# Kernel tuning notes

Measured on AMD Instinct MI355X. Metric: run time of the kernel, lower is better.

The kernel has to match this reference:

```python
import jax, jax.numpy as jnp
import numpy as np

B, L, D, H, DFF = 16, 2048, 256, 8, 1024
CYCLES = 2
DEP = D // H
EPS = 1e-6


def _mha(q, k, v, Wq, Wk, Wv, Wo, bo):
    # q: [N, Lq, D], k/v: [N, Lk, D]  (mask is None in the source for both calls)
    N, Lq, _ = q.shape
    Lk = k.shape[1]
    qh = (q @ Wq).reshape(N, Lq, H, DEP)
    kh = (k @ Wk).reshape(N, Lk, H, DEP)
    vh = (v @ Wv).reshape(N, Lk, H, DEP)
    logits = jnp.einsum('nqhd,nkhd->nhqk', qh, kh) / jnp.sqrt(jnp.float32(DEP))
    w = jax.nn.softmax(logits, axis=-1)
    o = jnp.einsum('nhqk,nkhd->nqhd', w, vh).reshape(N, Lq, D)
    return o @ Wo + bo


def _layernorm(x, g, b):
    mu = jnp.mean(x, axis=-1, keepdims=True)
    var = jnp.mean(jnp.square(x - mu), axis=-1, keepdims=True)
    return g * (x - mu) * jax.lax.rsqrt(var + EPS) + b


def setup_inputs() -> dict:
    key = jax.random.key(0)
    ks = jax.random.split(key, 10)
    sc = 1.0 / np.sqrt(D)
    return {
        'e': jax.random.normal(ks[0], (B, L, D), dtype=jnp.float32),
        'Wq': jax.random.normal(ks[1], (D, D), dtype=jnp.float32) * sc,
        'Wk': jax.random.normal(ks[2], (D, D), dtype=jnp.float32) * sc,
        'Wv': jax.random.normal(ks[3], (D, D), dtype=jnp.float32) * sc,
        'Wo': jax.random.normal(ks[4], (D, D), dtype=jnp.float32) * sc,
        'bo': jnp.zeros((D,), dtype=jnp.float32),
        'W1': jax.random.normal(ks[5], (D, DFF), dtype=jnp.float32) * sc,
        'b1': jnp.zeros((DFF,), dtype=jnp.float32),
        'W2': jax.random.normal(ks[6], (DFF, D), dtype=jnp.float32) * (1.0 / np.sqrt(DFF)),
        'b2': jnp.zeros((D,), dtype=jnp.float32),
        'g1': jnp.ones((D,), dtype=jnp.float32),
        'be1': jnp.zeros((D,), dtype=jnp.float32),
        'g2': jnp.ones((D,), dtype=jnp.float32),
        'be2': jnp.zeros((D,), dtype=jnp.float32),
        'training': False,
    }


def reference(e, Wq, Wk, Wv, Wo, bo, W1, b1, W2, b2, g1, be1, g2, be2, training):
    # training=False -> dropouts are identity (eval mode)
    b, l, d = e.shape
    h = e
    s = jnp.mean(h, axis=1)  # relay node [b, d]
    for _ in range(CYCLES):
        h_last = jnp.roll(h, -1, axis=1)  # cycle_shift(h, False)
        h_next = jnp.roll(h, 1, axis=1)   # cycle_shift(h, True)
        s_m = jnp.broadcast_to(s[:, None, :], h.shape)
        # context [b, l, 5, d] -> [b*l, 5, d]
        c = jnp.stack([h_last, h, h_next, e, s_m], axis=-2).reshape(b * l, 5, d)
        hq = h.reshape(b * l, 1, d)
        h = jax.nn.relu(_mha(hq, c, c, Wq, Wk, Wv, Wo, bo)).reshape(b, l, d)
        # relay attention (the source reuses multi_att_satellite weights here)
        sq = s[:, None, :]               # [b, 1, d]
        mc = jnp.concatenate([sq, h], axis=1)  # [b, l+1, d]
        s = jax.nn.relu(_mha(sq, mc, mc, Wq, Wk, Wv, Wo, bo)).reshape(b, d)
    out1 = _layernorm(e + h, g1, be1)
    ffn = jax.nn.relu(out1 @ W1 + b1) @ W2 + b2
    out2 = _layernorm(out1 + ffn, g2, be2)
    return out2, s
```

## Files before the change

### kernel.cpp

```cpp
#include <hip/hip_runtime.h>

typedef unsigned short u16;
typedef unsigned int u32;
typedef __attribute__((ext_vector_type(8))) short bf16x8;
typedef __attribute__((ext_vector_type(4))) float f32x4;

#define LCONST __launch_bounds__(256)

__device__ __forceinline__ u16 f2bf(float f) {
  u32 u = __float_as_uint(f);
  u32 r = (u + 0x7FFFu + ((u >> 16) & 1u)) >> 16;
  return (u16)r;
}
__device__ __forceinline__ float bflo(u32 w) { return __uint_as_float(w << 16); }
__device__ __forceinline__ float bfhi(u32 w) { return __uint_as_float(w & 0xFFFF0000u); }
__device__ __forceinline__ float b2f(u16 v) { return __uint_as_float(((u32)v) << 16); }

__device__ __forceinline__ float dot8(uint4 u, const float* q) {
  return q[0]*bflo(u.x) + q[1]*bfhi(u.x) + q[2]*bflo(u.y) + q[3]*bfhi(u.y)
       + q[4]*bflo(u.z) + q[5]*bfhi(u.z) + q[6]*bflo(u.w) + q[7]*bfhi(u.w);
}
__device__ __forceinline__ void fma8(uint4 u, float wt, float* a) {
  a[0] = fmaf(wt, bflo(u.x), a[0]); a[1] = fmaf(wt, bfhi(u.x), a[1]);
  a[2] = fmaf(wt, bflo(u.y), a[2]); a[3] = fmaf(wt, bfhi(u.y), a[3]);
  a[4] = fmaf(wt, bflo(u.z), a[4]); a[5] = fmaf(wt, bfhi(u.z), a[5]);
  a[6] = fmaf(wt, bflo(u.w), a[6]); a[7] = fmaf(wt, bfhi(u.w), a[7]);
}

__device__ __forceinline__ void gload16(const u16* g, u16* l) {
  __builtin_amdgcn_global_load_lds(
      (const __attribute__((address_space(1))) unsigned int*)g,
      (__attribute__((address_space(3))) unsigned int*)l, 16, 0, 0);
}

__global__ LCONST void prep_kernel(const float* __restrict__ e,
                                   const float* __restrict__ Wq, const float* __restrict__ Wk,
                                   const float* __restrict__ Wv, const float* __restrict__ Wo,
                                   const float* __restrict__ W1, const float* __restrict__ W2,
                                   u16* __restrict__ Wqkv_t, u16* __restrict__ Wo_t,
                                   u16* __restrict__ W1_t, u16* __restrict__ W2_t,
                                   float* __restrict__ part, u16* __restrict__ ebf) {
  int blk = blockIdx.x;
  int tid = threadIdx.x;
  if (blk < 3072) {
    int idx = blk * 256 + tid;
    if (idx < 196608) {
      int sub = idx >> 16, r = idx & 65535;
      int n = r >> 8, k = r & 255;
      const float* src = (sub == 0) ? Wq : ((sub == 1) ? Wk : Wv);
      Wqkv_t[idx] = f2bf(src[(size_t)k * 256 + n]);
    } else if (idx < 262144) {
      int r = idx - 196608;
      int n = r >> 8, k = r & 255;
      Wo_t[r] = f2bf(Wo[(size_t)k * 256 + n]);
    } else if (idx < 524288) {
      int r = idx - 262144;
      int n = r >> 8, k = r & 255;
      W1_t[r] = f2bf(W1[(size_t)k * 1024 + n]);
    } else {
      int r = idx - 524288;
      int n = r >> 10, k = r & 1023;
      W2_t[r] = f2bf(W2[(size_t)k * 256 + n]);
    }
  } else {
    int mb = blk - 3072;
    int b = mb >> 5, c = mb & 31;
    size_t base = ((size_t)b * 2048 + (size_t)c * 64) * 256 + tid;
    float s = 0.f;
    #pragma unroll 8
    for (int i = 0; i < 64; i++) {
      float v = e[base + (size_t)i * 256];
      s += v;
      ebf[base + (size_t)i * 256] = f2bf(v);
    }
    part[(size_t)mb * 256 + tid] = s;
  }
}

template <int BM, int BN, int EPI>
__global__ __launch_bounds__(512, (BM == 128) ? 4 : 6)
void gemm3_kernel(const u16* __restrict__ A, const u16* __restrict__ Bt,
                  const float* __restrict__ bias,
                  u16* __restrict__ C0, u16* __restrict__ C1, u16* __restrict__ C2,
                  const u16* __restrict__ resbf,
                  const float* __restrict__ g, const float* __restrict__ be,
                  float* __restrict__ Fout,
                  int M, int N, int K) {
  constexpr int WR = BM / 2;
  constexpr int MR = WR / 16;
  constexpr int ACH_PW = (BM / 8) / 8;
  constexpr int BCH_PW = 4;
  __shared__ __align__(16) u16 As[BM * 64];
  __shared__ __align__(16) u16 Bs[BN * 64];

  const int tid = threadIdx.x, lane = tid & 63, wid = tid >> 6;
  const int wm = wid >> 2, wn = wid & 3;

  const int ncol = N / BN;
  const int nwg = gridDim.x;
  const int bid = blockIdx.x;
  const int swz = (bid & 7) * (nwg >> 3) + (bid >> 3);
  const int mb = swz / ncol, nb = swz - mb * ncol;
  const int m0 = mb * BM, n0 = nb * BN;

  const int lrow8 = lane >> 3;
  const int cg = (lane & 7) ^ lrow8;

  f32x4 acc[MR][4] = {};
  for (int kt = 0; kt < K; kt += 64) {
    #pragma unroll
    for (int it = 0; it < ACH_PW; it++) {
      int ca = wid * ACH_PW + it;
      int row = ca * 8 + lrow8;
      gload16(A + (size_t)(m0 + row) * K + kt + cg * 8, (u16*)As + ca * 512);
    }
    #pragma unroll
    for (int it = 0; it < BCH_PW; it++) {
      int cb = wid * BCH_PW + it;
      int row = cb * 8 + lrow8;
      gload16(Bt + (size_t)(n0 + row) * K + kt + cg * 8, (u16*)Bs + cb * 512);
    }
    __syncthreads();
    const int lr = lane & 15, hi = lane >> 4;
    #pragma unroll
    for (int kk = 0; kk < 2; kk++) {
      const int slot = (kk * 4 + hi) ^ (lr & 7);
      bf16x8 af[MR], bfr[4];
      #pragma unroll
      for (int m = 0; m < MR; m++)
        af[m] = *(const bf16x8*)&As[(wm * WR + m * 16 + lr) * 64 + slot * 8];
      #pragma unroll
      for (int n = 0; n < 4; n++)
        bfr[n] = *(const bf16x8*)&Bs[(wn * 64 + n * 16 + lr) * 64 + slot * 8];
      #pragma unroll
      for (int m = 0; m < MR; m++)
        #pragma unroll
        for (int n = 0; n < 4; n++)
          acc[m][n] = __builtin_amdgcn_mfma_f32_16x16x32_bf16(af[m], bfr[n], acc[m][n], 0, 0, 0);
    }
    __syncthreads();
  }

  const int lr = lane & 15, hi = lane >> 4;
  if constexpr (EPI == 0) {
    const int bsel = n0 >> 8;
    u16* C = (bsel == 0) ? C0 : ((bsel == 1) ? C1 : C2);
    #pragma unroll
    for (int m = 0; m < MR; m++)
      #pragma unroll
      for (int n = 0; n < 4; n++)
        #pragma unroll
        for (int r = 0; r < 4; r++) {
          int row = m0 + wm * WR + m * 16 + hi * 4 + r;
          int col = wn * 64 + n * 16 + lr;
          C[(size_t)row * 256 + col] = f2bf(acc[m][n][r]);
        }
  } else if constexpr (EPI == 1) {
    #pragma unroll
    for (int m = 0; m < MR; m++)
      #pragma unroll
      for (int n = 0; n < 4; n++)
        #pragma unroll
        for (int r = 0; r < 4; r++) {
          int row = m0 + wm * WR + m * 16 + hi * 4 + r;
          int col = n0 + wn * 64 + n * 16 + lr;
          float v = fmaxf(acc[m][n][r] + bias[col], 0.f);
          C0[(size_t)row * N + col] = f2bf(v);
        }
  } else {
    __shared__ float rsum[BM], rsq[BM];
    if (tid < BM) { rsum[tid] = 0.f; rsq[tid] = 0.f; }
    __syncthreads();
    #pragma unroll
    for (int m = 0; m < MR; m++)
      #pragma unroll
      for (int n = 0; n < 4; n++)
        #pragma unroll
        for (int r = 0; r < 4; r++) {
          int rl = wm * WR + m * 16 + hi * 4 + r;
          int col = wn * 64 + n * 16 + lr;
          size_t gi = (size_t)(m0 + rl) * 256 + col;
          float v = acc[m][n][r] + bias[col];
          float x;
          if constexpr (EPI == 2) {
            v = fmaxf(v, 0.f);
            C0[gi] = f2bf(v);
            x = b2f(resbf[gi]) + v;
          } else {
            x = b2f(resbf[gi]) + v;
          }
          acc[m][n][r] = x;
        }
    #pragma unroll
    for (int m = 0; m < MR; m++)
      #pragma unroll
      for (int r = 0; r < 4; r++) {
        float s = 0.f, q = 0.f;
        #pragma unroll
        for (int n = 0; n < 4; n++) { float x = acc[m][n][r]; s += x; q += x * x; }
        #pragma unroll
        for (int off = 1; off < 16; off <<= 1) {
          s += __shfl_xor(s, off);
          q += __shfl_xor(q, off);
        }
        if (lr == 0) {
          int rl = wm * WR + m * 16 + hi * 4 + r;
          atomicAdd(&rsum[rl], s);
          atomicAdd(&rsq[rl], q);
        }
      }
    __syncthreads();
    #pragma unroll
    for (int m = 0; m < MR; m++)
      #pragma unroll
      for (int n = 0; n < 4; n++)
        #pragma unroll
        for (int r = 0; r < 4; r++) {
          int rl = wm * WR + m * 16 + hi * 4 + r;
          int col = wn * 64 + n * 16 + lr;
          size_t gi = (size_t)(m0 + rl) * 256 + col;
          float mu = rsum[rl] * (1.f / 256.f);
          float var = rsq[rl] * (1.f / 256.f) - mu * mu;
          float rstd = rsqrtf(fmaxf(var, 0.f) + 1e-6f);
          float o = g[col] * (acc[m][n][r] - mu) * rstd + be[col];
          if constexpr (EPI == 2) C1[gi] = f2bf(o);
          else                    Fout[gi] = o;
        }
  }
}

template <bool MEAN>
__global__ LCONST void proj_kernel(const float* __restrict__ X, const float* __restrict__ part,
                                   const float* __restrict__ Wq, const float* __restrict__ Wk,
                                   const float* __restrict__ Wv, float* __restrict__ Yq,
                                   float* __restrict__ Yk, float* __restrict__ Yv) {
  __shared__ float xs[256];
  __shared__ float red[256];
  const int b = blockIdx.x;
  const int wsel = blockIdx.y >> 2, n0 = (blockIdx.y & 3) * 64;
  const int tid = threadIdx.x;
  if constexpr (MEAN) {
    float s = 0.f;
    #pragma unroll
    for (int c = 0; c < 32; c++) s += part[((size_t)b * 32 + c) * 256 + tid];
    xs[tid] = s * (1.f / 2048.f);
  } else {
    xs[tid] = X[b * 256 + tid];
  }
  __syncthreads();
  const float* W = (wsel == 0) ? Wq : ((wsel == 1) ? Wk : Wv);
  float* Y = (wsel == 0) ? Yq : ((wsel == 1) ? Yk : Yv);
  const int c = tid & 63, g = tid >> 6;
  float p = 0.f;
  #pragma unroll 8
  for (int j = g * 64; j < g * 64 + 64; j++)
    p = fmaf(xs[j], W[(size_t)j * 256 + n0 + c], p);
  red[tid] = p;
  __syncthreads();
  if (g == 0)
    Y[b * 256 + n0 + c] = red[c] + red[64 + c] + red[128 + c] + red[192 + c];
}

__global__ LCONST void attn1_kernel(const u16* __restrict__ hq, const u16* __restrict__ pk,
                                    const u16* __restrict__ pv, const u16* __restrict__ ek,
                                    const u16* __restrict__ ev, const float* __restrict__ skp,
                                    const float* __restrict__ svp, u16* __restrict__ outp) {
  int t = blockIdx.x * 256 + threadIdx.x;
  int h = t & 7;
  size_t token = (size_t)(t >> 3);
  int b = (int)(token >> 11);
  int i = (int)(token & 2047);
  size_t tb = (size_t)b << 11;
  size_t ip = tb + ((i + 1) & 2047);
  size_t im = tb + ((i + 2047) & 2047);
  const int off = h * 32;

  float qf[32];
  {
    const u16* q = hq + token * 256 + off;
    #pragma unroll
    for (int c = 0; c < 4; c++) {
      uint4 u = *(const uint4*)(q + c * 8);
      qf[c*8+0] = bflo(u.x); qf[c*8+1] = bfhi(u.x);
      qf[c*8+2] = bflo(u.y); qf[c*8+3] = bfhi(u.y);
      qf[c*8+4] = bflo(u.z); qf[c*8+5] = bfhi(u.z);
      qf[c*8+6] = bflo(u.w); qf[c*8+7] = bfhi(u.w);
    }
  }
  const u16* kr0 = pk + ip * 256 + off;
  const u16* kr1 = pk + token * 256 + off;
  const u16* kr2 = pk + im * 256 + off;
  const u16* kr3 = ek + token * 256 + off;
  float lg[5];
  {
    float d0 = 0, d1 = 0, d2 = 0, d3 = 0;
    #pragma unroll
    for (int cc = 0; cc < 4; cc++) {
      d0 += dot8(*(const uint4*)(kr0 + cc * 8), qf + cc * 8);
      d1 += dot8(*(const uint4*)(kr1 + cc * 8), qf + cc * 8);
      d2 += dot8(*(const uint4*)(kr2 + cc * 8), qf + cc * 8);
      d3 += dot8(*(const uint4*)(kr3 + cc * 8), qf + cc * 8);
    }
    lg[0] = d0; lg[1] = d1; lg[2] = d2; lg[3] = d3;
    float d4 = 0;
    const float* s = skp + b * 256 + off;
    #pragma unroll
    for (int j = 0; j < 32; j++) d4 = fmaf(qf[j], s[j], d4);
    lg[4] = d4;
  }
  const float sc = 0.17677669529663687f;
  float m = lg[0];
  #pragma unroll
  for (int c = 1; c < 5; c++) m = fmaxf(m, lg[c]);
  float w[5], den = 0.f;
  #pragma unroll
  for (int c = 0; c < 5; c++) { w[c] = __expf((lg[c] - m) * sc); den += w[c]; }

  float a[32];
  #pragma unroll
  for (int j = 0; j < 32; j++) a[j] = 0.f;
  const u16* vr0 = pv + ip * 256 + off;
  const u16* vr1 = pv + token * 256 + off;
  const u16* vr2 = pv + im * 256 + off;
  const u16* vr3 = ev + token * 256 + off;
  #pragma unroll
  for (int cc = 0; cc < 4; cc++) {
    fma8(*(const uint4*)(vr0 + cc * 8), w[0], a + cc * 8);
    fma8(*(const uint4*)(vr1 + cc * 8), w[1], a + cc * 8);
    fma8(*(const uint4*)(vr2 + cc * 8), w[2], a + cc * 8);
    fma8(*(const uint4*)(vr3 + cc * 8), w[3], a + cc * 8);
  }
  {
    const float* s = svp + b * 256 + off;
    #pragma unroll
    for (int j = 0; j < 32; j++) a[j] = fmaf(w[4], s[j], a[j]);
  }
  float inv = 1.f / den;
  u16* o = outp + token * 256 + off;
  #pragma unroll
  for (int c = 0; c < 4; c++) {
    uint4 u;
    u.x = (u32)f2bf(a[c*8+0] * inv) | ((u32)f2bf(a[c*8+1] * inv) << 16);
    u.y = (u32)f2bf(a[c*8+2] * inv) | ((u32)f2bf(a[c*8+3] * inv) << 16);
    u.z = (u32)f2bf(a[c*8+4] * inv) | ((u32)f2bf(a[c*8+5] * inv) << 16);
    u.w = (u32)f2bf(a[c*8+6] * inv) | ((u32)f2bf(a[c*8+7] * inv) << 16);
    *(uint4*)(o + c * 8) = u;
  }
}

__global__ LCONST void mha2a_kernel(const float* __restrict__ sqp, const float* __restrict__ skp,
                                    const float* __restrict__ svp, const u16* __restrict__ pk,
                                    const u16* __restrict__ pv, float* __restrict__ partial) {
  __shared__ float rmax[4], rsum[4], racc[4][32];
  const int blk = blockIdx.x;
  const int bh = blk >> 2, c = blk & 3;
  const int b = bh >> 3, h = bh & 7;
  const int tid = threadIdx.x;
  const int lane = tid & 63, wid = tid >> 6;
  const int off = h * 32;
  const float sc = 0.17677669529663687f;

  float qf[32];
  {
    const float* q = sqp + b * 256 + off;
    #pragma unroll
    for (int j = 0; j < 32; j++) qf[j] = q[j];
  }
  const int k0 = c * 512 + tid;
  const int k1 = k0 + 256;
  const u16* kp0 = pk + ((size_t)b * 2048 + k0) * 256 + off;
  const u16* kp1 = pk + ((size_t)b * 2048 + k1) * 256 + off;
  float d0 = 0.f, d1 = 0.f;
  #pragma unroll
  for (int cc = 0; cc < 4; cc++) {
    d0 += dot8(*(const uint4*)(kp0 + cc * 8), qf + cc * 8);
    d1 += dot8(*(const uint4*)(kp1 + cc * 8), qf + cc * 8);
  }
  d0 *= sc; d1 *= sc;
  float ds = -1e30f;
  if (c == 0 && tid == 0) {
    float d = 0.f;
    const float* k = skp + b * 256 + off;
    #pragma unroll
    for (int j = 0; j < 32; j++) d = fmaf(qf[j], k[j], d);
    ds = d * sc;
  }
  float lmax = fmaxf(fmaxf(d0, d1), ds);
  #pragma unroll
  for (int o = 32; o; o >>= 1) lmax = fmaxf(lmax, __shfl_down(lmax, o));
  if (lane == 0) rmax[wid] = lmax;
  __syncthreads();
  const float M = fmaxf(fmaxf(rmax[0], rmax[1]), fmaxf(rmax[2], rmax[3]));

  float w0 = __expf(d0 - M), w1 = __expf(d1 - M);
  float lsum = w0 + w1;
  float a[32];
  #pragma unroll
  for (int j = 0; j < 32; j++) a[j] = 0.f;
  const u16* vp0 = pv + ((size_t)b * 2048 + k0) * 256 + off;
  const u16* vp1 = pv + ((size_t)b * 2048 + k1) * 256 + off;
  #pragma unroll
  for (int cc = 0; cc < 4; cc++) {
    fma8(*(const uint4*)(vp0 + cc * 8), w0, a + cc * 8);
    fma8(*(const uint4*)(vp1 + cc * 8), w1, a + cc * 8);
  }
  if (c == 0 && tid == 0) {
    float ws = __expf(ds - M);
    lsum += ws;
    const float* v = svp + b * 256 + off;
    #pragma unroll
    for (int j = 0; j < 32; j++) a[j] = fmaf(ws, v[j], a[j]);
  }
  #pragma unroll
  for (int o = 32; o; o >>= 1) lsum += __shfl_down(lsum, o);
  if (lane == 0) rsum[wid] = lsum;
  #pragma unroll
  for (int j = 0; j < 32; j++) {
    float v = a[j];
    #pragma unroll
    for (int o = 32; o; o >>= 1) v += __shfl_down(v, o);
    if (lane == 0) racc[wid][j] = v;
  }
  __syncthreads();
  float* P = partial + (size_t)blk * 36;
  if (tid < 32) {
    P[2 + tid] = racc[0][tid] + racc[1][tid] + racc[2][tid] + racc[3][tid];
    if (tid == 0) {
      P[0] = M;
      P[1] = rsum[0] + rsum[1] + rsum[2] + rsum[3];
    }
  }
}

__global__ LCONST void mha2c_kernel(const float* __restrict__ partial,
                                    const float* __restrict__ Wo, const float* __restrict__ bo,
                                    float* __restrict__ Y) {
  __shared__ float xs[256];
  __shared__ float red[256];
  const int b = blockIdx.x;
  const int n0 = blockIdx.y * 64;
  const int tid = threadIdx.x;
  {
    int hh = tid >> 5, d = tid & 31;
    const float* P = partial + (size_t)(b * 8 + hh) * 144;
    float M = fmaxf(fmaxf(P[0], P[36]), fmaxf(P[72], P[108]));
    float l = 0.f, o = 0.f;
    #pragma unroll
    for (int c = 0; c < 4; c++) {
      float f = __expf(P[c * 36] - M);
      l += f * P[c * 36 + 1];
      o += f * P[c * 36 + 2 + d];
    }
    xs[tid] = o / l;
  }
  __syncthreads();
  const int c = tid & 63, g = tid >> 6;
  float p = 0.f;
  #pragma unroll 8
  for (int j = g * 64; j < g * 64 + 64; j++)
    p = fmaf(xs[j], Wo[(size_t)j * 256 + n0 + c], p);
  red[tid] = p;
  __syncthreads();
  if (g == 0) {
    float v = red[c] + red[64 + c] + red[128 + c] + red[192 + c];
    Y[b * 256 + n0 + c] = fmaxf(v + bo[n0 + c], 0.f);
  }
}

extern "C" void kernel_launch(void* const* d_in, const int* in_sizes, int n_in,
                              void* d_out, int out_size, void* d_ws, size_t ws_size,
                              hipStream_t stream) {
  const float* e   = (const float*)d_in[0];
  const float* Wq  = (const float*)d_in[1];
  const float* Wk  = (const float*)d_in[2];
  const float* Wv  = (const float*)d_in[3];
  const float* Wo  = (const float*)d_in[4];
  const float* bo  = (const float*)d_in[5];
  const float* W1  = (const float*)d_in[6];
  const float* b1  = (const float*)d_in[7];
  const float* W2  = (const float*)d_in[8];
  const float* b2  = (const float*)d_in[9];
  const float* g1  = (const float*)d_in[10];
  const float* be1 = (const float*)d_in[11];
  const float* g2  = (const float*)d_in[12];
  const float* be2 = (const float*)d_in[13];

  char* wsb = (char*)d_ws;
  size_t off = 0;
  auto alc = [&](size_t n) { void* p = wsb + off; off += (n + 255) & ~(size_t)255; return p; };
  u16* Wqkv_t = (u16*)alc(768 * 256 * 2);
  u16* Wo_t   = (u16*)alc(65536 * 2);
  u16* W1_t   = (u16*)alc(262144 * 2);
  u16* W2_t   = (u16*)alc(262144 * 2);
  float* sB    = (float*)alc(4096 * 4);
  float* sqp   = (float*)alc(4096 * 4);
  float* skp   = (float*)alc(4096 * 4);
  float* svp   = (float*)alc(4096 * 4);
  float* partM = (float*)alc(512 * 36 * 4);
  float* part  = (float*)alc(524288);
  const size_t SZ = 16777216;
  u16* hq   = (u16*)alc(SZ);
  u16* ek   = (u16*)alc(SZ);
  u16* ev   = (u16*)alc(SZ);
  u16* pk   = (u16*)alc(SZ);
  u16* pv   = (u16*)alc(SZ);
  u16* ao   = (u16*)alc(SZ);
  u16* hbuf = (u16*)alc(SZ);
  u16* ebf  = (u16*)alc(SZ);
  u16* out1 = (u16*)alc(SZ);
  u16* ffn1 = hq;

  const int M = 32768;
  float* outp  = (float*)d_out;
  float* s_out = outp + 8388608;

  prep_kernel<<<3584, 256, 0, stream>>>(e, Wq, Wk, Wv, Wo, W1, W2,
      Wqkv_t, Wo_t, W1_t, W2_t, part, ebf);

  proj_kernel<true><<<dim3(16, 12), 256, 0, stream>>>(nullptr, part, Wq, Wk, Wv, sqp, skp, svp);
  gemm3_kernel<128, 256, 0><<<768, 512, 0, stream>>>(ebf, Wqkv_t, nullptr, hq, ek, ev,
      nullptr, nullptr, nullptr, nullptr, M, 768, 256);
  attn1_kernel<<<1024, 256, 0, stream>>>(hq, ek, ev, ek, ev, skp, svp, ao);
  gemm3_kernel<64, 256, 1><<<512, 512, 0, stream>>>(ao, Wo_t, bo, hbuf, nullptr, nullptr,
      nullptr, nullptr, nullptr, nullptr, M, 256, 256);
  gemm3_kernel<128, 256, 0><<<768, 512, 0, stream>>>(hbuf, Wqkv_t, nullptr, hq, pk, pv,
      nullptr, nullptr, nullptr, nullptr, M, 768, 256);
  mha2a_kernel<<<512, 256, 0, stream>>>(sqp, skp, svp, pk, pv, partM);
  mha2c_kernel<<<dim3(16, 4), 256, 0, stream>>>(partM, Wo, bo, sB);
  proj_kernel<false><<<dim3(16, 12), 256, 0, stream>>>(sB, nullptr, Wq, Wk, Wv, sqp, skp, svp);

  attn1_kernel<<<1024, 256, 0, stream>>>(hq, pk, pv, ek, ev, skp, svp, ao);
  gemm3_kernel<64, 256, 2><<<512, 512, 0, stream>>>(ao, Wo_t, bo, hbuf, out1, nullptr,
      ebf, g1, be1, nullptr, M, 256, 256);
  gemm3_kernel<128, 256, 0><<<512, 512, 0, stream>>>(hbuf, Wqkv_t + 65536, nullptr, pk, pv, nullptr,
      nullptr, nullptr, nullptr, nullptr, M, 512, 256);
  mha2a_kernel<<<512, 256, 0, stream>>>(sqp, skp, svp, pk, pv, partM);
  mha2c_kernel<<<dim3(16, 4), 256, 0, stream>>>(partM, Wo, bo, s_out);

  gemm3_kernel<128, 256, 1><<<1024, 512, 0, stream>>>(out1, W1_t, b1, ffn1, nullptr, nullptr,
      nullptr, nullptr, nullptr, nullptr, M, 1024, 256);
  gemm3_kernel<64, 256, 4><<<512, 512, 0, stream>>>(ffn1, W2_t, b2, nullptr, nullptr, nullptr,
      out1, g2, be2, outp, M, 256, 1024);
  (void)in_sizes; (void)n_in; (void)out_size; (void)ws_size;
}
```

Baseline: 278.5 us.

## Fuse FFN up-projection, ReLU, down-projection and LayerNorm into one kernel

```diff
diff --git a/kernel.cpp b/kernel.cpp
--- a/kernel.cpp
+++ b/kernel.cpp
@@ -181,14 +181,9 @@
           int col = wn * 64 + n * 16 + lr;
           size_t gi = (size_t)(m0 + rl) * 256 + col;
           float v = acc[m][n][r] + bias[col];
-          float x;
-          if constexpr (EPI == 2) {
-            v = fmaxf(v, 0.f);
-            C0[gi] = f2bf(v);
-            x = b2f(resbf[gi]) + v;
-          } else {
-            x = b2f(resbf[gi]) + v;
-          }
+          v = fmaxf(v, 0.f);
+          C0[gi] = f2bf(v);
+          float x = b2f(resbf[gi]) + v;
           acc[m][n][r] = x;
         }
     #pragma unroll
@@ -223,10 +218,154 @@
           float var = rsq[rl] * (1.f / 256.f) - mu * mu;
           float rstd = rsqrtf(fmaxf(var, 0.f) + 1e-6f);
           float o = g[col] * (acc[m][n][r] - mu) * rstd + be[col];
-          if constexpr (EPI == 2) C1[gi] = f2bf(o);
-          else                    Fout[gi] = o;
-        }
-  }
+          C1[gi] = f2bf(o);
+        }
+  }
+}
+
+__global__ __launch_bounds__(512, 2)
+void ffn_fused_kernel(const u16* __restrict__ out1, const u16* __restrict__ W1_t,
+                      const float* __restrict__ b1, const u16* __restrict__ W2_t,
+                      const float* __restrict__ b2, const float* __restrict__ g,
+                      const float* __restrict__ be, float* __restrict__ Fout) {
+  __shared__ __align__(16) u16 As[128 * 64];
+  __shared__ __align__(16) u16 Bs[256 * 64];
+  __shared__ __align__(16) u16 Cs[128 * 256];
+  const int tid = threadIdx.x, lane = tid & 63, wid = tid >> 6;
+  const int wm = wid >> 2, wn = wid & 3;
+  const int nwg = gridDim.x, bid = blockIdx.x;
+  const int swz = (bid & 7) * (nwg >> 3) + (bid >> 3);
+  const int m0 = swz * 128;
+  const int lrow8 = lane >> 3;
+  const int cg = (lane & 7) ^ lrow8;
+  const int lr = lane & 15, hi = lane >> 4;
+
+  f32x4 acc2[4][4] = {};
+  for (int nb = 0; nb < 4; nb++) {
+    f32x4 acc1[4][4] = {};
+    for (int kt = 0; kt < 4; kt++) {
+      #pragma unroll
+      for (int it = 0; it < 2; it++) {
+        int ca = wid * 2 + it;
+        int row = ca * 8 + lrow8;
+        gload16(out1 + (size_t)(m0 + row) * 256 + kt * 64 + cg * 8, (u16*)As + ca * 512);
+      }
+      #pragma unroll
+      for (int it = 0; it < 4; it++) {
+        int cb = wid * 4 + it;
+        int row = cb * 8 + lrow8;
+        gload16(W1_t + (size_t)(nb * 256 + row) * 256 + kt * 64 + cg * 8, (u16*)Bs + cb * 512);
+      }
+      __syncthreads();
+      #pragma unroll
+      for (int kk = 0; kk < 2; kk++) {
+        const int slot = (kk * 4 + hi) ^ (lr & 7);
+        bf16x8 af[4], bfr[4];
+        #pragma unroll
+        for (int m = 0; m < 4; m++)
+          af[m] = *(const bf16x8*)&As[(wm * 64 + m * 16 + lr) * 64 + slot * 8];
+        #pragma unroll
+        for (int n = 0; n < 4; n++)
+          bfr[n] = *(const bf16x8*)&Bs[(wn * 64 + n * 16 + lr) * 64 + slot * 8];
+        #pragma unroll
+        for (int m = 0; m < 4; m++)
+          #pragma unroll
+          for (int n = 0; n < 4; n++)
+            acc1[m][n] = __builtin_amdgcn_mfma_f32_16x16x32_bf16(af[m], bfr[n], acc1[m][n], 0, 0, 0);
+      }
+      __syncthreads();
+    }
+    #pragma unroll
+    for (int m = 0; m < 4; m++)
+      #pragma unroll
+      for (int n = 0; n < 4; n++)
+        #pragma unroll
+        for (int r = 0; r < 4; r++) {
+          int rl = wm * 64 + m * 16 + hi * 4 + r;
+          int col = wn * 64 + n * 16 + lr;
+          float v = fmaxf(acc1[m][n][r] + b1[nb * 256 + col], 0.f);
+          int s = col >> 3;
+          int sp = (s & 24) | ((s & 7) ^ (rl & 7));
+          Cs[rl * 256 + sp * 8 + (col & 7)] = f2bf(v);
+        }
+    __syncthreads();
+    for (int kt2 = 0; kt2 < 4; kt2++) {
+      #pragma unroll
+      for (int it = 0; it < 4; it++) {
+        int cb = wid * 4 + it;
+        int row = cb * 8 + lrow8;
+        gload16(W2_t + (size_t)row * 1024 + nb * 256 + kt2 * 64 + cg * 8, (u16*)Bs + cb * 512);
+      }
+      __syncthreads();
+      #pragma unroll
+      for (int kk = 0; kk < 2; kk++) {
+        const int j = kk * 4 + hi;
+        bf16x8 af[4], bfr[4];
+        #pragma unroll
+        for (int m = 0; m < 4; m++) {
+          int row = wm * 64 + m * 16 + lr;
+          af[m] = *(const bf16x8*)&Cs[row * 256 + (kt2 * 8 + (j ^ (row & 7))) * 8];
+        }
+        #pragma unroll
+        for (int n = 0; n < 4; n++)
+          bfr[n] = *(const bf16x8*)&Bs[(wn * 64 + n * 16 + lr) * 64 + ((j ^ (lr & 7))) * 8];
+        #pragma unroll
+        for (int m = 0; m < 4; m++)
+          #pragma unroll
+          for (int n = 0; n < 4; n++)
+            acc2[m][n] = __builtin_amdgcn_mfma_f32_16x16x32_bf16(af[m], bfr[n], acc2[m][n], 0, 0, 0);
+      }
+      __syncthreads();
+    }
+  }
+  float* rsum = (float*)As;
+  float* rsq  = rsum + 128;
+  if (tid < 128) { rsum[tid] = 0.f; rsq[tid] = 0.f; }
+  __syncthreads();
+  #pragma unroll
+  for (int m = 0; m < 4; m++)
+    #pragma unroll
+    for (int n = 0; n < 4; n++)
+      #pragma unroll
+      for (int r = 0; r < 4; r++) {
+        int rl = wm * 64 + m * 16 + hi * 4 + r;
+        int col = wn * 64 + n * 16 + lr;
+        size_t gi = (size_t)(m0 + rl) * 256 + col;
+        acc2[m][n][r] = acc2[m][n][r] + b2[col] + b2f(out1[gi]);
+      }
+  #pragma unroll
+  for (int m = 0; m < 4; m++)
+    #pragma unroll
+    for (int r = 0; r < 4; r++) {
+      float s = 0.f, q = 0.f;
+      #pragma unroll
+      for (int n = 0; n < 4; n++) { float x = acc2[m][n][r]; s += x; q += x * x; }
+      #pragma unroll
+      for (int off = 1; off < 16; off <<= 1) {
+        s += __shfl_xor(s, off);
+        q += __shfl_xor(q, off);
+      }
+      if (lr == 0) {
+        int rl = wm * 64 + m * 16 + hi * 4 + r;
+        atomicAdd(&rsum[rl], s);
+        atomicAdd(&rsq[rl], q);
+      }
+    }
+  __syncthreads();
+  #pragma unroll
+  for (int m = 0; m < 4; m++)
+    #pragma unroll
+    for (int n = 0; n < 4; n++)
+      #pragma unroll
+      for (int r = 0; r < 4; r++) {
+        int rl = wm * 64 + m * 16 + hi * 4 + r;
+        int col = wn * 64 + n * 16 + lr;
+        size_t gi = (size_t)(m0 + rl) * 256 + col;
+        float mu = rsum[rl] * (1.f / 256.f);
+        float var = rsq[rl] * (1.f / 256.f) - mu * mu;
+        float rstd = rsqrtf(fmaxf(var, 0.f) + 1e-6f);
+        Fout[gi] = g[col] * (acc2[m][n][r] - mu) * rstd + be[col];
+      }
 }
 
 template <bool MEAN>
@@ -508,7 +647,6 @@
   u16* hbuf = (u16*)alc(SZ);
   u16* ebf  = (u16*)alc(SZ);
   u16* out1 = (u16*)alc(SZ);
-  u16* ffn1 = hq;
 
   const int M = 32768;
   float* outp  = (float*)d_out;
@@ -537,9 +675,6 @@
   mha2a_kernel<<<512, 256, 0, stream>>>(sqp, skp, svp, pk, pv, partM);
   mha2c_kernel<<<dim3(16, 4), 256, 0, stream>>>(partM, Wo, bo, s_out);
 
-  gemm3_kernel<128, 256, 1><<<1024, 512, 0, stream>>>(out1, W1_t, b1, ffn1, nullptr, nullptr,
-      nullptr, nullptr, nullptr, nullptr, M, 1024, 256);
-  gemm3_kernel<64, 256, 4><<<512, 512, 0, stream>>>(ffn1, W2_t, b2, nullptr, nullptr, nullptr,
-      out1, g2, be2, outp, M, 256, 1024);
+  ffn_fused_kernel<<<256, 512, 0, stream>>>(out1, W1_t, b1, W2_t, b2, g2, be2, outp);
   (void)in_sizes; (void)n_in; (void)out_size; (void)ws_size;
 }
```

New measurement: 322.9 us. +15.9%, slower.

## Add persistent-A GEMM looping over N blocks and fuse relay output with projection

Applied to the files above, without the earlier changes.

```diff
diff --git a/kernel.cpp b/kernel.cpp
--- a/kernel.cpp
+++ b/kernel.cpp
@@ -77,8 +77,88 @@
   }
 }
 
+template <int NCOL, int EPI>
+__global__ __launch_bounds__(512, 4)
+void gemmP_kernel(const u16* __restrict__ A, const u16* __restrict__ Bt,
+                  const float* __restrict__ bias,
+                  u16* __restrict__ C0, u16* __restrict__ C1, u16* __restrict__ C2) {
+  __shared__ __align__(16) u16 As[64 * 256];
+  __shared__ __align__(16) u16 Bs[256 * 64];
+  const int tid = threadIdx.x, lane = tid & 63, wid = tid >> 6;
+  const int wm = wid >> 2, wn = wid & 3;
+  const int nwg = gridDim.x, bid = blockIdx.x;
+  const int swz = (bid & 7) * (nwg >> 3) + (bid >> 3);
+  const int m0 = swz * 64;
+  const int lrow8 = lane >> 3;
+  const int cg = (lane & 7) ^ lrow8;
+  const int lr = lane & 15, hi = lane >> 4;
+
+  #pragma unroll
+  for (int kt = 0; kt < 4; kt++) {
+    int row = wid * 8 + lrow8;
+    gload16(A + (size_t)(m0 + row) * 256 + kt * 64 + cg * 8,
+            (u16*)As + kt * 4096 + wid * 512);
+  }
+
+  for (int nb = 0; nb < NCOL; nb++) {
+    f32x4 acc[2][4] = {};
+    for (int kt = 0; kt < 4; kt++) {
+      #pragma unroll
+      for (int it = 0; it < 4; it++) {
+        int cb = wid * 4 + it;
+        int row = cb * 8 + lrow8;
+        gload16(Bt + (size_t)(nb * 256 + row) * 256 + kt * 64 + cg * 8,
+                (u16*)Bs + cb * 512);
+      }
+      __syncthreads();
+      #pragma unroll
+      for (int kk = 0; kk < 2; kk++) {
+        const int slot = (kk * 4 + hi) ^ (lr & 7);
+        bf16x8 af[2], bfr[4];
+        #pragma unroll
+        for (int m = 0; m < 2; m++)
+          af[m] = *(const bf16x8*)&As[kt * 4096 + (wm * 32 + m * 16 + lr) * 64 + slot * 8];
+        #pragma unroll
+        for (int n = 0; n < 4; n++)
+          bfr[n] = *(const bf16x8*)&Bs[(wn * 64 + n * 16 + lr) * 64 + slot * 8];
+        #pragma unroll
+        for (int m = 0; m < 2; m++)
+          #pragma unroll
+          for (int n = 0; n < 4; n++)
+            acc[m][n] = __builtin_amdgcn_mfma_f32_16x16x32_bf16(af[m], bfr[n], acc[m][n], 0, 0, 0);
+      }
+      __syncthreads();
+    }
+    if constexpr (EPI == 0) {
+      u16* C = (nb == 0) ? C0 : ((nb == 1) ? C1 : C2);
+      #pragma unroll
+      for (int m = 0; m < 2; m++)
+        #pragma unroll
+        for (int n = 0; n < 4; n++)
+          #pragma unroll
+          for (int r = 0; r < 4; r++) {
+            int row = m0 + wm * 32 + m * 16 + hi * 4 + r;
+            int col = wn * 64 + n * 16 + lr;
+            C[(size_t)row * 256 + col] = f2bf(acc[m][n][r]);
+          }
+    } else {
+      #pragma unroll
+      for (int m = 0; m < 2; m++)
+        #pragma unroll
+        for (int n = 0; n < 4; n++)
+          #pragma unroll
+          for (int r = 0; r < 4; r++) {
+            int row = m0 + wm * 32 + m * 16 + hi * 4 + r;
+            int col = nb * 256 + wn * 64 + n * 16 + lr;
+            float v = fmaxf(acc[m][n][r] + bias[col], 0.f);
+            C0[(size_t)row * (NCOL * 256) + col] = f2bf(v);
+          }
+    }
+  }
+}
+
 template <int BM, int BN, int EPI>
-__global__ __launch_bounds__(512, (BM == 128) ? 4 : 6)
+__global__ __launch_bounds__(512, 6)
 void gemm3_kernel(const u16* __restrict__ A, const u16* __restrict__ Bt,
                   const float* __restrict__ bias,
                   u16* __restrict__ C0, u16* __restrict__ C1, u16* __restrict__ C2,
@@ -142,20 +222,7 @@
   }
 
   const int lr = lane & 15, hi = lane >> 4;
-  if constexpr (EPI == 0) {
-    const int bsel = n0 >> 8;
-    u16* C = (bsel == 0) ? C0 : ((bsel == 1) ? C1 : C2);
-    #pragma unroll
-    for (int m = 0; m < MR; m++)
-      #pragma unroll
-      for (int n = 0; n < 4; n++)
-        #pragma unroll
-        for (int r = 0; r < 4; r++) {
-          int row = m0 + wm * WR + m * 16 + hi * 4 + r;
-          int col = wn * 64 + n * 16 + lr;
-          C[(size_t)row * 256 + col] = f2bf(acc[m][n][r]);
-        }
-  } else if constexpr (EPI == 1) {
+  if constexpr (EPI == 1) {
     #pragma unroll
     for (int m = 0; m < MR; m++)
       #pragma unroll
@@ -465,6 +532,52 @@
     float v = red[c] + red[64 + c] + red[128 + c] + red[192 + c];
     Y[b * 256 + n0 + c] = fmaxf(v + bo[n0 + c], 0.f);
   }
+}
+
+__global__ LCONST void mha2cp_kernel(const float* __restrict__ partial,
+                                     const float* __restrict__ Wo, const float* __restrict__ bo,
+                                     const float* __restrict__ Wq, const float* __restrict__ Wk,
+                                     const float* __restrict__ Wv,
+                                     float* __restrict__ Yq, float* __restrict__ Yk,
+                                     float* __restrict__ Yv) {
+  __shared__ float xs[256];
+  __shared__ float ss[256];
+  __shared__ float red[256];
+  const int b = blockIdx.x;
+  const int wsel = blockIdx.y >> 2, n0 = (blockIdx.y & 3) * 64;
+  const int tid = threadIdx.x;
+  {
+    int hh = tid >> 5, d = tid & 31;
+    const float* P = partial + (size_t)(b * 8 + hh) * 144;
+    float M = fmaxf(fmaxf(P[0], P[36]), fmaxf(P[72], P[108]));
+    float l = 0.f, o = 0.f;
+    #pragma unroll
+    for (int c = 0; c < 4; c++) {
+      float f = __expf(P[c * 36] - M);
+      l += f * P[c * 36 + 1];
+      o += f * P[c * 36 + 2 + d];
+    }
+    xs[tid] = o / l;
+  }
+  __syncthreads();
+  {
+    float a = 0.f;
+    #pragma unroll 8
+    for (int j = 0; j < 256; j++) a = fmaf(xs[j], Wo[(size_t)j * 256 + tid], a);
+    ss[tid] = fmaxf(a + bo[tid], 0.f);
+  }
+  __syncthreads();
+  const float* W = (wsel == 0) ? Wq : ((wsel == 1) ? Wk : Wv);
+  float* Y = (wsel == 0) ? Yq : ((wsel == 1) ? Yk : Yv);
+  const int c = tid & 63, g = tid >> 6;
+  float p = 0.f;
+  #pragma unroll 8
+  for (int j = g * 64; j < g * 64 + 64; j++)
+    p = fmaf(ss[j], W[(size_t)j * 256 + n0 + c], p);
+  red[tid] = p;
+  __syncthreads();
+  if (g == 0)
+    Y[b * 256 + n0 + c] = red[c] + red[64 + c] + red[128 + c] + red[192 + c];
 }
 
 extern "C" void kernel_launch(void* const* d_in, const int* in_sizes, int n_in,
@@ -492,7 +605,6 @@
   u16* Wo_t   = (u16*)alc(65536 * 2);
   u16* W1_t   = (u16*)alc(262144 * 2);
   u16* W2_t   = (u16*)alc(262144 * 2);
-  float* sB    = (float*)alc(4096 * 4);
   float* sqp   = (float*)alc(4096 * 4);
   float* skp   = (float*)alc(4096 * 4);
   float* svp   = (float*)alc(4096 * 4);
@@ -518,27 +630,22 @@
       Wqkv_t, Wo_t, W1_t, W2_t, part, ebf);
 
   proj_kernel<true><<<dim3(16, 12), 256, 0, stream>>>(nullptr, part, Wq, Wk, Wv, sqp, skp, svp);
-  gemm3_kernel<128, 256, 0><<<768, 512, 0, stream>>>(ebf, Wqkv_t, nullptr, hq, ek, ev,
-      nullptr, nullptr, nullptr, nullptr, M, 768, 256);
+  gemmP_kernel<3, 0><<<512, 512, 0, stream>>>(ebf, Wqkv_t, nullptr, hq, ek, ev);
   attn1_kernel<<<1024, 256, 0, stream>>>(hq, ek, ev, ek, ev, skp, svp, ao);
   gemm3_kernel<64, 256, 1><<<512, 512, 0, stream>>>(ao, Wo_t, bo, hbuf, nullptr, nullptr,
       nullptr, nullptr, nullptr, nullptr, M, 256, 256);
-  gemm3_kernel<128, 256, 0><<<768, 512, 0, stream>>>(hbuf, Wqkv_t, nullptr, hq, pk, pv,
-      nullptr, nullptr, nullptr, nullptr, M, 768, 256);
+  gemmP_kernel<3, 0><<<512, 512, 0, stream>>>(hbuf, Wqkv_t, nullptr, hq, pk, pv);
   mha2a_kernel<<<512, 256, 0, stream>>>(sqp, skp, svp, pk, pv, partM);
-  mha2c_kernel<<<dim3(16, 4), 256, 0, stream>>>(partM, Wo, bo, sB);
-  proj_kernel<false><<<dim3(16, 12), 256, 0, stream>>>(sB, nullptr, Wq, Wk, Wv, sqp, skp, svp);
+  mha2cp_kernel<<<dim3(16, 12), 256, 0, stream>>>(partM, Wo, bo, Wq, Wk, Wv, sqp, skp, svp);
 
   attn1_kernel<<<1024, 256, 0, stream>>>(hq, pk, pv, ek, ev, skp, svp, ao);
   gemm3_kernel<64, 256, 2><<<512, 512, 0, stream>>>(ao, Wo_t, bo, hbuf, out1, nullptr,
       ebf, g1, be1, nullptr, M, 256, 256);
-  gemm3_kernel<128, 256, 0><<<512, 512, 0, stream>>>(hbuf, Wqkv_t + 65536, nullptr, pk, pv, nullptr,
-      nullptr, nullptr, nullptr, nullptr, M, 512, 256);
+  gemmP_kernel<2, 0><<<512, 512, 0, stream>>>(hbuf, Wqkv_t + 65536, nullptr, pk, pv, nullptr);
   mha2a_kernel<<<512, 256, 0, stream>>>(sqp, skp, svp, pk, pv, partM);
   mha2c_kernel<<<dim3(16, 4), 256, 0, stream>>>(partM, Wo, bo, s_out);
 
-  gemm3_kernel<128, 256, 1><<<1024, 512, 0, stream>>>(out1, W1_t, b1, ffn1, nullptr, nullptr,
-      nullptr, nullptr, nullptr, nullptr, M, 1024, 256);
+  gemmP_kernel<4, 1><<<512, 512, 0, stream>>>(out1, W1_t, b1, ffn1, nullptr, nullptr);
   gemm3_kernel<64, 256, 4><<<512, 512, 0, stream>>>(ffn1, W2_t, b2, nullptr, nullptr, nullptr,
       out1, g2, be2, outp, M, 256, 1024);
   (void)in_sizes; (void)n_in; (void)out_size; (void)ws_size;
```

Result: slower. 291.5 us (+4.7%).

## Fuse per-token 5-way attention with Wo projection GEMM into one kernel

Applied to the files above, without the earlier changes.

```diff
diff --git a/kernel.cpp b/kernel.cpp
--- a/kernel.cpp
+++ b/kernel.cpp
@@ -180,16 +180,7 @@
           int rl = wm * WR + m * 16 + hi * 4 + r;
           int col = wn * 64 + n * 16 + lr;
           size_t gi = (size_t)(m0 + rl) * 256 + col;
-          float v = acc[m][n][r] + bias[col];
-          float x;
-          if constexpr (EPI == 2) {
-            v = fmaxf(v, 0.f);
-            C0[gi] = f2bf(v);
-            x = b2f(resbf[gi]) + v;
-          } else {
-            x = b2f(resbf[gi]) + v;
-          }
-          acc[m][n][r] = x;
+          acc[m][n][r] = acc[m][n][r] + bias[col] + b2f(resbf[gi]);
         }
     #pragma unroll
     for (int m = 0; m < MR; m++)
@@ -222,9 +213,209 @@
           float mu = rsum[rl] * (1.f / 256.f);
           float var = rsq[rl] * (1.f / 256.f) - mu * mu;
           float rstd = rsqrtf(fmaxf(var, 0.f) + 1e-6f);
-          float o = g[col] * (acc[m][n][r] - mu) * rstd + be[col];
-          if constexpr (EPI == 2) C1[gi] = f2bf(o);
-          else                    Fout[gi] = o;
+          Fout[gi] = g[col] * (acc[m][n][r] - mu) * rstd + be[col];
+        }
+  }
+}
+
+template <int EPI>
+__global__ __launch_bounds__(512, 4)
+void attnwo_kernel(const u16* __restrict__ hq, const u16* __restrict__ pk,
+                   const u16* __restrict__ pv, const u16* __restrict__ ek,
+                   const u16* __restrict__ ev, const float* __restrict__ skp,
+                   const float* __restrict__ svp,
+                   const u16* __restrict__ Wo_t, const float* __restrict__ bo,
+                   u16* __restrict__ C0, u16* __restrict__ C1,
+                   const u16* __restrict__ resbf,
+                   const float* __restrict__ g, const float* __restrict__ be) {
+  __shared__ __align__(16) u16 As[64 * 256];
+  __shared__ __align__(16) u16 Bs[256 * 64];
+  const int tid = threadIdx.x, lane = tid & 63, wid = tid >> 6;
+  const int wm = wid >> 2, wn = wid & 3;
+  const int nwg = gridDim.x, bid = blockIdx.x;
+  const int swz = (bid & 7) * (nwg >> 3) + (bid >> 3);
+  const int m0 = swz * 64;
+
+  {
+    const int r = tid >> 3, h = tid & 7;
+    const size_t token = (size_t)(m0 + r);
+    const int b = (int)(token >> 11);
+    const int i = (int)(token & 2047);
+    const size_t tb = (size_t)b << 11;
+    const size_t ip = tb + ((i + 1) & 2047);
+    const size_t im = tb + ((i + 2047) & 2047);
+    const int off = h * 32;
+
+    float qf[32];
+    {
+      const u16* q = hq + token * 256 + off;
+      #pragma unroll
+      for (int c = 0; c < 4; c++) {
+        uint4 u = *(const uint4*)(q + c * 8);
+        qf[c*8+0] = bflo(u.x); qf[c*8+1] = bfhi(u.x);
+        qf[c*8+2] = bflo(u.y); qf[c*8+3] = bfhi(u.y);
+        qf[c*8+4] = bflo(u.z); qf[c*8+5] = bfhi(u.z);
+        qf[c*8+6] = bflo(u.w); qf[c*8+7] = bfhi(u.w);
+      }
+    }
+    const u16* kr0 = pk + ip * 256 + off;
+    const u16* kr1 = pk + token * 256 + off;
+    const u16* kr2 = pk + im * 256 + off;
+    const u16* kr3 = ek + token * 256 + off;
+    float lg[5];
+    {
+      float d0 = 0, d1 = 0, d2 = 0, d3 = 0;
+      #pragma unroll
+      for (int cc = 0; cc < 4; cc++) {
+        d0 += dot8(*(const uint4*)(kr0 + cc * 8), qf + cc * 8);
+        d1 += dot8(*(const uint4*)(kr1 + cc * 8), qf + cc * 8);
+        d2 += dot8(*(const uint4*)(kr2 + cc * 8), qf + cc * 8);
+        d3 += dot8(*(const uint4*)(kr3 + cc * 8), qf + cc * 8);
+      }
+      lg[0] = d0; lg[1] = d1; lg[2] = d2; lg[3] = d3;
+      float d4 = 0;
+      const float* s = skp + b * 256 + off;
+      #pragma unroll
+      for (int j = 0; j < 32; j++) d4 = fmaf(qf[j], s[j], d4);
+      lg[4] = d4;
+    }
+    const float sc = 0.17677669529663687f;
+    float mx = lg[0];
+    #pragma unroll
+    for (int c = 1; c < 5; c++) mx = fmaxf(mx, lg[c]);
+    float w[5], den = 0.f;
+    #pragma unroll
+    for (int c = 0; c < 5; c++) { w[c] = __expf((lg[c] - mx) * sc); den += w[c]; }
+
+    float a[32];
+    #pragma unroll
+    for (int j = 0; j < 32; j++) a[j] = 0.f;
+    const u16* vr0 = pv + ip * 256 + off;
+    const u16* vr1 = pv + token * 256 + off;
+    const u16* vr2 = pv + im * 256 + off;
+    const u16* vr3 = ev + token * 256 + off;
+    #pragma unroll
+    for (int cc = 0; cc < 4; cc++) {
+      fma8(*(const uint4*)(vr0 + cc * 8), w[0], a + cc * 8);
+      fma8(*(const uint4*)(vr1 + cc * 8), w[1], a + cc * 8);
+      fma8(*(const uint4*)(vr2 + cc * 8), w[2], a + cc * 8);
+      fma8(*(const uint4*)(vr3 + cc * 8), w[3], a + cc * 8);
+    }
+    {
+      const float* s = svp + b * 256 + off;
+      #pragma unroll
+      for (int j = 0; j < 32; j++) a[j] = fmaf(w[4], s[j], a[j]);
+    }
+    const float inv = 1.f / den;
+    #pragma unroll
+    for (int c = 0; c < 4; c++) {
+      uint4 u;
+      u.x = (u32)f2bf(a[c*8+0] * inv) | ((u32)f2bf(a[c*8+1] * inv) << 16);
+      u.y = (u32)f2bf(a[c*8+2] * inv) | ((u32)f2bf(a[c*8+3] * inv) << 16);
+      u.z = (u32)f2bf(a[c*8+4] * inv) | ((u32)f2bf(a[c*8+5] * inv) << 16);
+      u.w = (u32)f2bf(a[c*8+6] * inv) | ((u32)f2bf(a[c*8+7] * inv) << 16);
+      int s = h * 4 + c;
+      int sp = (s & 24) | ((s & 7) ^ (r & 7));
+      *(uint4*)&As[r * 256 + sp * 8] = u;
+    }
+  }
+  __syncthreads();
+
+  const int lrow8 = lane >> 3;
+  const int cg = (lane & 7) ^ lrow8;
+  const int lr = lane & 15, hi = lane >> 4;
+  f32x4 acc[2][4] = {};
+  for (int kt = 0; kt < 4; kt++) {
+    #pragma unroll
+    for (int it = 0; it < 4; it++) {
+      int cb = wid * 4 + it;
+      int row = cb * 8 + lrow8;
+      gload16(Wo_t + (size_t)row * 256 + kt * 64 + cg * 8, (u16*)Bs + cb * 512);
+    }
+    __syncthreads();
+    #pragma unroll
+    for (int kk = 0; kk < 2; kk++) {
+      bf16x8 af[2], bfr[4];
+      #pragma unroll
+      for (int m = 0; m < 2; m++) {
+        int row = wm * 32 + m * 16 + lr;
+        int sp = kt * 8 + ((kk * 4 + hi) ^ (row & 7));
+        af[m] = *(const bf16x8*)&As[row * 256 + sp * 8];
+      }
+      const int slotB = (kk * 4 + hi) ^ (lr & 7);
+      #pragma unroll
+      for (int n = 0; n < 4; n++)
+        bfr[n] = *(const bf16x8*)&Bs[(wn * 64 + n * 16 + lr) * 64 + slotB * 8];
+      #pragma unroll
+      for (int m = 0; m < 2; m++)
+        #pragma unroll
+        for (int n = 0; n < 4; n++)
+          acc[m][n] = __builtin_amdgcn_mfma_f32_16x16x32_bf16(af[m], bfr[n], acc[m][n], 0, 0, 0);
+    }
+    __syncthreads();
+  }
+
+  if constexpr (EPI == 1) {
+    #pragma unroll
+    for (int m = 0; m < 2; m++)
+      #pragma unroll
+      for (int n = 0; n < 4; n++)
+        #pragma unroll
+        for (int r = 0; r < 4; r++) {
+          int row = m0 + wm * 32 + m * 16 + hi * 4 + r;
+          int col = wn * 64 + n * 16 + lr;
+          float v = fmaxf(acc[m][n][r] + bo[col], 0.f);
+          C0[(size_t)row * 256 + col] = f2bf(v);
+        }
+  } else {
+    __shared__ float rsum[64], rsq[64];
+    if (tid < 64) { rsum[tid] = 0.f; rsq[tid] = 0.f; }
+    __syncthreads();
+    #pragma unroll
+    for (int m = 0; m < 2; m++)
+      #pragma unroll
+      for (int n = 0; n < 4; n++)
+        #pragma unroll
+        for (int r = 0; r < 4; r++) {
+          int rl = wm * 32 + m * 16 + hi * 4 + r;
+          int col = wn * 64 + n * 16 + lr;
+          size_t gi = (size_t)(m0 + rl) * 256 + col;
+          float v = fmaxf(acc[m][n][r] + bo[col], 0.f);
+          C0[gi] = f2bf(v);
+          acc[m][n][r] = b2f(resbf[gi]) + v;
+        }
+    #pragma unroll
+    for (int m = 0; m < 2; m++)
+      #pragma unroll
+      for (int r = 0; r < 4; r++) {
+        float s = 0.f, q = 0.f;
+        #pragma unroll
+        for (int n = 0; n < 4; n++) { float x = acc[m][n][r]; s += x; q += x * x; }
+        #pragma unroll
+        for (int off = 1; off < 16; off <<= 1) {
+          s += __shfl_xor(s, off);
+          q += __shfl_xor(q, off);
+        }
+        if (lr == 0) {
+          int rl = wm * 32 + m * 16 + hi * 4 + r;
+          atomicAdd(&rsum[rl], s);
+          atomicAdd(&rsq[rl], q);
+        }
+      }
+    __syncthreads();
+    #pragma unroll
+    for (int m = 0; m < 2; m++)
+      #pragma unroll
+      for (int n = 0; n < 4; n++)
+        #pragma unroll
+        for (int r = 0; r < 4; r++) {
+          int rl = wm * 32 + m * 16 + hi * 4 + r;
+          int col = wn * 64 + n * 16 + lr;
+          size_t gi = (size_t)(m0 + rl) * 256 + col;
+          float mu = rsum[rl] * (1.f / 256.f);
+          float var = rsq[rl] * (1.f / 256.f) - mu * mu;
+          float rstd = rsqrtf(fmaxf(var, 0.f) + 1e-6f);
+          C1[gi] = f2bf(g[col] * (acc[m][n][r] - mu) * rstd + be[col]);
         }
   }
 }
@@ -259,93 +450,6 @@
   __syncthreads();
   if (g == 0)
     Y[b * 256 + n0 + c] = red[c] + red[64 + c] + red[128 + c] + red[192 + c];
-}
-
-__global__ LCONST void attn1_kernel(const u16* __restrict__ hq, const u16* __restrict__ pk,
-                                    const u16* __restrict__ pv, const u16* __restrict__ ek,
-                                    const u16* __restrict__ ev, const float* __restrict__ skp,
-                                    const float* __restrict__ svp, u16* __restrict__ outp) {
-  int t = blockIdx.x * 256 + threadIdx.x;
-  int h = t & 7;
-  size_t token = (size_t)(t >> 3);
-  int b = (int)(token >> 11);
-  int i = (int)(token & 2047);
-  size_t tb = (size_t)b << 11;
-  size_t ip = tb + ((i + 1) & 2047);
-  size_t im = tb + ((i + 2047) & 2047);
-  const int off = h * 32;
-
-  float qf[32];
-  {
-    const u16* q = hq + token * 256 + off;
-    #pragma unroll
-    for (int c = 0; c < 4; c++) {
-      uint4 u = *(const uint4*)(q + c * 8);
-      qf[c*8+0] = bflo(u.x); qf[c*8+1] = bfhi(u.x);
-      qf[c*8+2] = bflo(u.y); qf[c*8+3] = bfhi(u.y);
-      qf[c*8+4] = bflo(u.z); qf[c*8+5] = bfhi(u.z);
-      qf[c*8+6] = bflo(u.w); qf[c*8+7] = bfhi(u.w);
-    }
-  }
-  const u16* kr0 = pk + ip * 256 + off;
-  const u16* kr1 = pk + token * 256 + off;
-  const u16* kr2 = pk + im * 256 + off;
-  const u16* kr3 = ek + token * 256 + off;
-  float lg[5];
-  {
-    float d0 = 0, d1 = 0, d2 = 0, d3 = 0;
-    #pragma unroll
-    for (int cc = 0; cc < 4; cc++) {
-      d0 += dot8(*(const uint4*)(kr0 + cc * 8), qf + cc * 8);
-      d1 += dot8(*(const uint4*)(kr1 + cc * 8), qf + cc * 8);
-      d2 += dot8(*(const uint4*)(kr2 + cc * 8), qf + cc * 8);
-      d3 += dot8(*(const uint4*)(kr3 + cc * 8), qf + cc * 8);
-    }
-    lg[0] = d0; lg[1] = d1; lg[2] = d2; lg[3] = d3;
-    float d4 = 0;
-    const float* s = skp + b * 256 + off;
-    #pragma unroll
-    for (int j = 0; j < 32; j++) d4 = fmaf(qf[j], s[j], d4);
-    lg[4] = d4;
-  }
-  const float sc = 0.17677669529663687f;
-  float m = lg[0];
-  #pragma unroll
-  for (int c = 1; c < 5; c++) m = fmaxf(m, lg[c]);
-  float w[5], den = 0.f;
-  #pragma unroll
-  for (int c = 0; c < 5; c++) { w[c] = __expf((lg[c] - m) * sc); den += w[c]; }
-
-  float a[32];
-  #pragma unroll
-  for (int j = 0; j < 32; j++) a[j] = 0.f;
-  const u16* vr0 = pv + ip * 256 + off;
-  const u16* vr1 = pv + token * 256 + off;
-  const u16* vr2 = pv + im * 256 + off;
-  const u16* vr3 = ev + token * 256 + off;
-  #pragma unroll
-  for (int cc = 0; cc < 4; cc++) {
-    fma8(*(const uint4*)(vr0 + cc * 8), w[0], a + cc * 8);
-    fma8(*(const uint4*)(vr1 + cc * 8), w[1], a + cc * 8);
-    fma8(*(const uint4*)(vr2 + cc * 8), w[2], a + cc * 8);
-    fma8(*(const uint4*)(vr3 + cc * 8), w[3], a + cc * 8);
-  }
-  {
-    const float* s = svp + b * 256 + off;
-    #pragma unroll
-    for (int j = 0; j < 32; j++) a[j] = fmaf(w[4], s[j], a[j]);
-  }
-  float inv = 1.f / den;
-  u16* o = outp + token * 256 + off;
-  #pragma unroll
-  for (int c = 0; c < 4; c++) {
-    uint4 u;
-    u.x = (u32)f2bf(a[c*8+0] * inv) | ((u32)f2bf(a[c*8+1] * inv) << 16);
-    u.y = (u32)f2bf(a[c*8+2] * inv) | ((u32)f2bf(a[c*8+3] * inv) << 16);
-    u.z = (u32)f2bf(a[c*8+4] * inv) | ((u32)f2bf(a[c*8+5] * inv) << 16);
-    u.w = (u32)f2bf(a[c*8+6] * inv) | ((u32)f2bf(a[c*8+7] * inv) << 16);
-    *(uint4*)(o + c * 8) = u;
-  }
 }
 
 __global__ LCONST void mha2a_kernel(const float* __restrict__ sqp, const float* __restrict__ skp,
@@ -504,7 +608,6 @@
   u16* ev   = (u16*)alc(SZ);
   u16* pk   = (u16*)alc(SZ);
   u16* pv   = (u16*)alc(SZ);
-  u16* ao   = (u16*)alc(SZ);
   u16* hbuf = (u16*)alc(SZ);
   u16* ebf  = (u16*)alc(SZ);
   u16* out1 = (u16*)alc(SZ);
@@ -520,18 +623,16 @@
   proj_kernel<true><<<dim3(16, 12), 256, 0, stream>>>(nullptr, part, Wq, Wk, Wv, sqp, skp, svp);
   gemm3_kernel<128, 256, 0><<<768, 512, 0, stream>>>(ebf, Wqkv_t, nullptr, hq, ek, ev,
       nullptr, nullptr, nullptr, nullptr, M, 768, 256);
-  attn1_kernel<<<1024, 256, 0, stream>>>(hq, ek, ev, ek, ev, skp, svp, ao);
-  gemm3_kernel<64, 256, 1><<<512, 512, 0, stream>>>(ao, Wo_t, bo, hbuf, nullptr, nullptr,
-      nullptr, nullptr, nullptr, nullptr, M, 256, 256);
+  attnwo_kernel<1><<<512, 512, 0, stream>>>(hq, ek, ev, ek, ev, skp, svp,
+      Wo_t, bo, hbuf, nullptr, nullptr, nullptr, nullptr);
   gemm3_kernel<128, 256, 0><<<768, 512, 0, stream>>>(hbuf, Wqkv_t, nullptr, hq, pk, pv,
       nullptr, nullptr, nullptr, nullptr, M, 768, 256);
   mha2a_kernel<<<512, 256, 0, stream>>>(sqp, skp, svp, pk, pv, partM);
   mha2c_kernel<<<dim3(16, 4), 256, 0, stream>>>(partM, Wo, bo, sB);
   proj_kernel<false><<<dim3(16, 12), 256, 0, stream>>>(sB, nullptr, Wq, Wk, Wv, sqp, skp, svp);
 
-  attn1_kernel<<<1024, 256, 0, stream>>>(hq, pk, pv, ek, ev, skp, svp, ao);
-  gemm3_kernel<64, 256, 2><<<512, 512, 0, stream>>>(ao, Wo_t, bo, hbuf, out1, nullptr,
-      ebf, g1, be1, nullptr, M, 256, 256);
+  attnwo_kernel<2><<<512, 512, 0, stream>>>(hq, pk, pv, ek, ev, skp, svp,
+      Wo_t, bo, hbuf, out1, ebf, g1, be1);
   gemm3_kernel<128, 256, 0><<<512, 512, 0, stream>>>(hbuf, Wqkv_t + 65536, nullptr, pk, pv, nullptr,
       nullptr, nullptr, nullptr, nullptr, M, 512, 256);
   mha2a_kernel<<<512, 256, 0, stream>>>(sqp, skp, svp, pk, pv, partM);
```

Result: faster. 258.5 us (median of 2 runs) (-7.2%).
